# Kernel tuning notes

Hardware: AMD Instinct MI355X
Metric: run time of the kernel (lower is better)

## Reference

```python
import jax, jax.numpy as jnp
import numpy as np

H = 256      # hid_dim
HEADS = 4
DH = H // HEADS
B = 256      # batch
L = 128      # route_max_len (all routes full length)
T = 256      # max_trg_len
ID = 50000   # id_size
IN_DIM = H + 1  # emb + rate


def setup_inputs() -> dict:
    key = jax.random.key(0)
    ks = jax.random.split(key, 20)
    # bidirectional chain edges per sample, with node offsets pre-applied
    j = np.arange(L - 1)
    s = np.concatenate([j, j + 1]); d = np.concatenate([j + 1, j])
    off = (np.arange(B) * L)[:, None]
    edge_index = jnp.asarray(np.stack([(s[None] + off).reshape(-1),
                                       (d[None] + off).reshape(-1)]), dtype=jnp.int64)
    sc = 0.05
    inp = dict(
        route_emb=jax.random.normal(ks[0], (B, L, H), jnp.float32),
        edge_index=edge_index,
        trg_id=jax.random.randint(ks[1], (T, B), 0, ID),
        trg_rate=jax.random.uniform(ks[2], (T, B, 1), jnp.float32),
        routes=jax.random.randint(ks[3], (L, B), 0, ID),
        route_attn_mask=jnp.ones((B, L), jnp.int32),
        # parameters
        emb_id=jax.random.normal(ks[4], (ID, H), jnp.float32) * sc,
        gat_w=jax.random.normal(ks[5], (H, H), jnp.float32) * sc,
        gat_a_src=jax.random.normal(ks[6], (HEADS, DH), jnp.float32) * sc,
        gat_a_dst=jax.random.normal(ks[7], (HEADS, DH), jnp.float32) * sc,
        gat_bias=jnp.zeros((H,), jnp.float32),
        ln_gamma=jnp.ones((H,), jnp.float32),
        ln_beta=jnp.zeros((H,), jnp.float32),
        gru_w_ih=jax.random.normal(ks[8], (3 * H, IN_DIM), jnp.float32) * sc,
        gru_w_hh=jax.random.normal(ks[9], (3 * H, H), jnp.float32) * sc,
        gru_b_ih=jnp.zeros((3 * H,), jnp.float32),
        gru_b_hh=jnp.zeros((3 * H,), jnp.float32),
        fc1_w=jax.random.normal(ks[10], (2 * H, 2 * H), jnp.float32) * sc,
        fc1_b=jnp.zeros((2 * H,), jnp.float32),
        fc2_w=jax.random.normal(ks[11], (1, 2 * H), jnp.float32) * sc,
        fc2_b=jnp.zeros((1,), jnp.float32),
    )
    return inp


def _layernorm(x, g, b, eps=1e-5):
    m = jnp.mean(x, -1, keepdims=True)
    v = jnp.var(x, -1, keepdims=True)
    return (x - m) * jax.lax.rsqrt(v + eps) * g + b


def _gat(x, edge_index, W, a_src, a_dst, bias):
    # PyG GATConv, concat=True, add_self_loops=False, eval mode (no dropout)
    N = x.shape[0]
    xw = (x @ W).reshape(N, HEADS, DH)                   # [N,heads,dh]
    src, dst = edge_index[0], edge_index[1]
    a_s = jnp.sum(xw * a_src, -1)                        # [N,heads]
    a_d = jnp.sum(xw * a_dst, -1)
    e = a_s[src] + a_d[dst]                              # [E,heads]
    e = jnp.where(e > 0, e, 0.2 * e)                     # LeakyReLU(0.2)
    e_max = jax.ops.segment_max(e, dst, num_segments=N)
    ex = jnp.exp(e - e_max[dst])
    denom = jax.ops.segment_sum(ex, dst, num_segments=N)
    alpha = ex / (denom[dst] + 1e-16)                    # softmax per dst node
    out = jax.ops.segment_sum(xw[src] * alpha[:, :, None], dst, num_segments=N)
    return out.reshape(N, H) + bias


def _forward(route_emb, trg_rate, emb_id, gat_w, gat_a_src, gat_a_dst, gat_bias,
             ln_gamma, ln_beta, gru_w_ih, gru_w_hh, gru_b_ih, gru_b_hh,
             fc1_w, fc1_b, fc2_w, fc2_b,
             edge_index, trg_id, routes, route_attn_mask):
    # ---- RouteGraphEncoder (all routes have valid_len == L) ----
    nodes = route_emb.reshape(B * L, H)
    h_new = _gat(nodes, edge_index, gat_w, gat_a_src, gat_a_dst, gat_bias)
    h = _layernorm(nodes + h_new, ln_gamma, ln_beta)
    route_outputs = h.reshape(B, L, H)                    # [B,L,H]
    # initial decoder hidden: masked mean over route positions
    hidden0 = jnp.mean(route_outputs, axis=1)             # [B,H]

    mask = route_attn_mask                                # [B,L] int
    inv_sqrt = 1.0 / jnp.sqrt(jnp.float32(H))

    def gru_cell(x, hprev):
        gi = x @ gru_w_ih.T + gru_b_ih                    # [B,3H]
        gh = hprev @ gru_w_hh.T + gru_b_hh
        ir, iz, inn = jnp.split(gi, 3, -1)
        hr, hz, hn = jnp.split(gh, 3, -1)
        r = jax.nn.sigmoid(ir + hr)
        z = jax.nn.sigmoid(iz + hz)
        n = jnp.tanh(inn + r * hn)
        return (1.0 - z) * n + z * hprev

    def step(hprev, xs):
        tid, trate = xs                                   # [B], [B,1]
        x = jnp.concatenate([emb_id[tid], trate], -1)     # [B,H+1]
        hnew = gru_cell(x, hprev)
        scores = jnp.einsum('bh,blh->bl', hnew, route_outputs) * inv_sqrt
        scores = jnp.where(mask == 0, -1e9, scores)
        attn = jax.nn.softmax(scores, -1)                 # [B,L]
        weighted = jnp.einsum('bl,blh->bh', attn, route_outputs)
        pred_id = jnp.where(mask == 0, 0.0, attn)         # masked_fill(mask==0,0)
        rate_in = jnp.concatenate([hnew, weighted], -1)   # [B,2H]
        pred_rate = jax.nn.sigmoid(
            jax.nn.relu(rate_in @ fc1_w.T + fc1_b) @ fc2_w.T + fc2_b)  # [B,1]
        return hnew, (pred_id, pred_rate)

    # teacher forcing ratio = 1.0: input at step t is trg_id[t-1]
    xs = (trg_id[:-1], trg_rate[:-1])
    _, (ids, rates) = jax.lax.scan(step, hidden0, xs)     # [T-1,B,L],[T-1,B,1]
    outputs_id = jnp.concatenate([jnp.zeros((1, B, L), ids.dtype), ids], 0)
    outputs_rate = jnp.concatenate([jnp.zeros((1, B, 1), rates.dtype), rates], 0)
    # trg_len == T for all samples -> mask_trg is all ones (no-op)
    return outputs_id, outputs_rate


def reference(route_emb, edge_index, trg_id, trg_rate, routes, route_attn_mask,
              emb_id, gat_w, gat_a_src, gat_a_dst, gat_bias, ln_gamma, ln_beta,
              gru_w_ih, gru_w_hh, gru_b_ih, gru_b_hh, fc1_w, fc1_b, fc2_w, fc2_b):
    return _forward(route_emb, trg_rate, emb_id, gat_w, gat_a_src, gat_a_dst,
                    gat_bias, ln_gamma, ln_beta, gru_w_ih, gru_w_hh, gru_b_ih,
                    gru_b_hh, fc1_w, fc1_b, fc2_w, fc2_b,
                    edge_index, trg_id, routes, route_attn_mask)
```

## Files before the change

### kernel.cpp

```cpp
#include <hip/hip_runtime.h>
#include <math.h>

#define RATE_OFF 8388608

#define O_XW    0
#define O_SC    0
#define O_AS    8388608
#define O_AD    8519680
#define O_RO    8650752
#define O_HSEQ  17039360
#define O_H16   33882112
#define O_GI16  42303488
#define O_WE16  45449216
#define O_RACC  53805056
#define O_WIH16 53870336
#define O_FC116 53968640

typedef _Float16 half_t;
typedef __attribute__((ext_vector_type(2))) _Float16 half2_t;
typedef __attribute__((ext_vector_type(4))) _Float16 half4_t;
typedef __attribute__((ext_vector_type(8))) _Float16 half8_t;
typedef __attribute__((ext_vector_type(4))) float f32x4;

__global__ void k_misc_zero(float* __restrict__ out, float* __restrict__ racc) {
  int i = blockIdx.x * 256 + threadIdx.x;
  if (i < 32768) out[i] = 0.f;
  else if (i < 33024) out[RATE_OFF + (i - 32768)] = 0.f;
  else racc[i - 33024] = 0.f;
}

__global__ void k_cvt_w(const float* __restrict__ wih, const float* __restrict__ fc1,
                        half_t* __restrict__ wih16, half_t* __restrict__ fc116) {
  int i = blockIdx.x * 256 + threadIdx.x;
  if (i < 196608) {
    int n = i >> 8, k = i & 255;
    wih16[i] = (half_t)wih[n * 257 + k];
  } else {
    int j = i - 196608;
    fc116[j] = (half_t)fc1[j];
  }
}

__global__ __launch_bounds__(256) void k_gemm_xw(const float* __restrict__ A,
    const float* __restrict__ B, float* __restrict__ C) {
  __shared__ float As[16 * 68], Bs[16 * 68];
  const int tid = threadIdx.x;
  const int m0 = blockIdx.y * 64, n0 = blockIdx.x * 64;
  const int ty = tid >> 4, tx = tid & 15;
  const int am = tid >> 2, ak = (tid & 3) * 4;
  const int bk = tid >> 4, bn = (tid & 15) * 4;
  float c[4][4] = {};
  for (int k0 = 0; k0 < 256; k0 += 16) {
    float4 av = *(const float4*)&A[(size_t)(m0 + am) * 256 + k0 + ak];
    As[(ak + 0) * 68 + am] = av.x;
    As[(ak + 1) * 68 + am] = av.y;
    As[(ak + 2) * 68 + am] = av.z;
    As[(ak + 3) * 68 + am] = av.w;
    *(float4*)&Bs[bk * 68 + bn] = *(const float4*)&B[(size_t)(k0 + bk) * 256 + n0 + bn];
    __syncthreads();
#pragma unroll
    for (int kk = 0; kk < 16; ++kk) {
      float4 a = *(const float4*)&As[kk * 68 + ty * 4];
      float4 b = *(const float4*)&Bs[kk * 68 + tx * 4];
      float aa[4] = {a.x, a.y, a.z, a.w};
      float bb[4] = {b.x, b.y, b.z, b.w};
#pragma unroll
      for (int i = 0; i < 4; ++i)
#pragma unroll
        for (int j = 0; j < 4; ++j) c[i][j] += aa[i] * bb[j];
    }
    __syncthreads();
  }
  for (int i = 0; i < 4; ++i) {
    float4 v = make_float4(c[i][0], c[i][1], c[i][2], c[i][3]);
    *(float4*)&C[(size_t)(m0 + ty * 4 + i) * 256 + n0 + tx * 4] = v;
  }
}

__global__ void k_asd(const float* __restrict__ xw, const float* __restrict__ asrc,
                      const float* __restrict__ adst, float* __restrict__ a_s,
                      float* __restrict__ a_d) {
  int g = blockIdx.x * 256 + threadIdx.x;
  int n = g >> 2, h = g & 3;
  const float* row = &xw[(size_t)n * 256 + h * 64];
  float s1 = 0.f, s2 = 0.f;
  for (int d = 0; d < 64; ++d) {
    float v = row[d];
    s1 += v * asrc[h * 64 + d];
    s2 += v * adst[h * 64 + d];
  }
  a_s[g] = s1;
  a_d[g] = s2;
}

__global__ __launch_bounds__(256) void k_gat_ln(const float* __restrict__ xw,
    const float* __restrict__ a_s, const float* __restrict__ a_d,
    const float* __restrict__ bias, const float* __restrict__ nodes,
    const float* __restrict__ gamma, const float* __restrict__ beta,
    float* __restrict__ ro) {
  __shared__ float rs[4], rq[4];
  const int n = blockIdx.x, c = threadIdx.x, h = c >> 6;
  const int p = n & 127;
  const bool h1 = (p > 0), h2 = (p < 127);
  const float ad = a_d[n * 4 + h];
  float e1 = -1e30f, e2 = -1e30f;
  if (h1) { float e = a_s[(n - 1) * 4 + h] + ad; e1 = (e > 0.f) ? e : 0.2f * e; }
  if (h2) { float e = a_s[(n + 1) * 4 + h] + ad; e2 = (e > 0.f) ? e : 0.2f * e; }
  const float mx = fmaxf(e1, e2);
  const float x1 = h1 ? expf(e1 - mx) : 0.f;
  const float x2 = h2 ? expf(e2 - mx) : 0.f;
  const float inv = 1.f / (x1 + x2 + 1e-16f);
  float o = 0.f;
  if (h1) o += x1 * inv * xw[(size_t)(n - 1) * 256 + c];
  if (h2) o += x2 * inv * xw[(size_t)(n + 1) * 256 + c];
  o += bias[c];
  const float t = nodes[(size_t)n * 256 + c] + o;
  float sv = t, qv = t * t;
  for (int off = 32; off; off >>= 1) { sv += __shfl_down(sv, off); qv += __shfl_down(qv, off); }
  if ((c & 63) == 0) { rs[c >> 6] = sv; rq[c >> 6] = qv; }
  __syncthreads();
  const float S = rs[0] + rs[1] + rs[2] + rs[3];
  const float Q = rq[0] + rq[1] + rq[2] + rq[3];
  const float mean = S * (1.f / 256.f);
  const float var = Q * (1.f / 256.f) - mean * mean;
  ro[(size_t)n * 256 + c] = (t - mean) * rsqrtf(var + 1e-5f) * gamma[c] + beta[c];
}

__global__ void k_hidden0(const float* __restrict__ ro, float* __restrict__ hseq) {
  int b = blockIdx.x, c = threadIdx.x;
  float s = 0.f;
  for (int l = 0; l < 128; ++l) s += ro[(size_t)(b * 128 + l) * 256 + c];
  hseq[(size_t)b * 256 + c] = s * (1.f / 128.f);
}

__global__ __launch_bounds__(256) void k_gi_mfma(const float* __restrict__ emb,
    const int* __restrict__ tgid, const float* __restrict__ trate,
    const half_t* __restrict__ wih16, const float* __restrict__ wih,
    const float* __restrict__ bih, half_t* __restrict__ gi16, int s0) {
  const int tid = threadIdx.x;
  const int wave = tid >> 6, lane = tid & 63;
  const int q = lane >> 4, ln = lane & 15;
  const int m0 = blockIdx.y * 64;
  const int nw = blockIdx.x * 256 + wave * 64;
  const float* aptr[4];
#pragma unroll
  for (int mt = 0; mt < 4; ++mt) {
    const int mr = m0 + mt * 16 + ln;
    const int sl = mr >> 8, b = mr & 255;
    const int id = tgid[(s0 + sl) * 256 + b];
    aptr[mt] = emb + (size_t)id * 256;
  }
  f32x4 acc[4][4] = {};
  for (int kc = 0; kc < 8; ++kc) {
    const int k0 = kc * 32;
    const int kq = k0 + q * 8;
    half8_t a[4], bfr[4];
#pragma unroll
    for (int mt = 0; mt < 4; ++mt) {
      float4 f0 = *(const float4*)(aptr[mt] + kq);
      float4 f1 = *(const float4*)(aptr[mt] + kq + 4);
      half8_t v;
      v[0] = (half_t)f0.x; v[1] = (half_t)f0.y; v[2] = (half_t)f0.z; v[3] = (half_t)f0.w;
      v[4] = (half_t)f1.x; v[5] = (half_t)f1.y; v[6] = (half_t)f1.z; v[7] = (half_t)f1.w;
      a[mt] = v;
    }
#pragma unroll
    for (int nt = 0; nt < 4; ++nt) {
      const int n = nw + nt * 16 + ln;
      bfr[nt] = *(const half8_t*)(wih16 + (size_t)n * 256 + kq);
    }
#pragma unroll
    for (int mt = 0; mt < 4; ++mt)
#pragma unroll
      for (int nt = 0; nt < 4; ++nt)
        acc[mt][nt] = __builtin_amdgcn_mfma_f32_16x16x32_f16(a[mt], bfr[nt], acc[mt][nt], 0, 0, 0);
  }
  float wr[4], bb[4];
#pragma unroll
  for (int nt = 0; nt < 4; ++nt) {
    const int n = nw + nt * 16 + ln;
    wr[nt] = wih[(size_t)n * 257 + 256];
    bb[nt] = bih[n];
  }
#pragma unroll
  for (int mt = 0; mt < 4; ++mt) {
#pragma unroll
    for (int i = 0; i < 4; ++i) {
      const int mr2 = m0 + mt * 16 + q * 4 + i;
      const int sl = mr2 >> 8, b = mr2 & 255;
      const float tr = trate[(s0 + sl) * 256 + b];
#pragma unroll
      for (int nt = 0; nt < 4; ++nt) {
        const int n = nw + nt * 16 + ln;
        gi16[(size_t)mr2 * 768 + n] = (half_t)(acc[mt][nt][i] + tr * wr[nt] + bb[nt]);
      }
    }
  }
}

__global__ __launch_bounds__(768, 3) void k_scan(const float* __restrict__ whh,
    const half_t* __restrict__ gi16, const float* __restrict__ bhh,
    float* __restrict__ hseq, half_t* __restrict__ h16, int s0, int ns) {
  __shared__ half2_t h2[128];
  __shared__ float hf[256];
  __shared__ float gsum[768];
  const int tid = threadIdx.x;
  const int b = blockIdx.x;
  half2_t w[128];
  const float* wrow = &whh[(size_t)tid * 256];
#pragma unroll
  for (int i = 0; i < 64; ++i) {
    float4 v = *(const float4*)&wrow[i * 4];
    half2_t p0, p1;
    p0.x = (half_t)v.x; p0.y = (half_t)v.y;
    p1.x = (half_t)v.z; p1.y = (half_t)v.w;
    w[2 * i] = p0;
    w[2 * i + 1] = p1;
  }
  const float bh = bhh[tid];
  if (tid < 256) {
    float hv = hseq[(size_t)s0 * 65536 + (size_t)b * 256 + tid];
    hf[tid] = hv;
    ((half_t*)h2)[tid] = (half_t)hv;
  }
  __syncthreads();
  for (int sl = 0; sl < ns; ++sl) {
    float gr = 0.f, gz = 0.f, gn = 0.f;
    if (tid < 256) {
      const half_t* gis = &gi16[((size_t)sl * 256 + b) * 768];
      gr = (float)gis[tid]; gz = (float)gis[256 + tid]; gn = (float)gis[512 + tid];
    }
    float acc = bh;
#pragma unroll
    for (int i = 0; i < 128; ++i) {
#if __has_builtin(__builtin_amdgcn_fdot2)
      acc = __builtin_amdgcn_fdot2(h2[i], w[i], acc, false);
#else
      half2_t hv = h2[i], wv = w[i];
      acc += (float)hv.x * (float)wv.x + (float)hv.y * (float)wv.y;
#endif
    }
    gsum[tid] = acc;
    __syncthreads();
    if (tid < 256) {
      const float r = 1.f / (1.f + expf(-(gr + gsum[tid])));
      const float z = 1.f / (1.f + expf(-(gz + gsum[256 + tid])));
      const float nn = tanhf(gn + r * gsum[512 + tid]);
      const float hn = (1.f - z) * nn + z * hf[tid];
      hf[tid] = hn;
      ((half_t*)h2)[tid] = (half_t)hn;
      hseq[(size_t)(s0 + sl + 1) * 65536 + (size_t)b * 256 + tid] = hn;
      h16[(size_t)(s0 + sl + 1) * 65536 + (size_t)b * 256 + tid] = (half_t)hn;
    }
    __syncthreads();
  }
}

__global__ __launch_bounds__(256) void k_scores(const float* __restrict__ hseq,
    const float* __restrict__ ro, float* __restrict__ sc) {
  __shared__ float As[16 * 68], Bs[16 * 68];
  const int tid = threadIdx.x;
  const int l0 = blockIdx.x * 64, s0 = blockIdx.y * 64, b = blockIdx.z;
  const int ty = tid >> 4, tx = tid & 15;
  const int am = tid >> 2, ak = (tid & 3) * 4;
  const float* hrow = &hseq[(size_t)(s0 + am + 1) * 65536 + (size_t)b * 256];
  const float* brow = &ro[(size_t)b * 32768 + (size_t)(l0 + am) * 256];
  float c[4][4] = {};
  for (int k0 = 0; k0 < 256; k0 += 16) {
    float4 av = *(const float4*)&hrow[k0 + ak];
    As[(ak + 0) * 68 + am] = av.x;
    As[(ak + 1) * 68 + am] = av.y;
    As[(ak + 2) * 68 + am] = av.z;
    As[(ak + 3) * 68 + am] = av.w;
    float4 bv = *(const float4*)&brow[k0 + ak];
    Bs[(ak + 0) * 68 + am] = bv.x;
    Bs[(ak + 1) * 68 + am] = bv.y;
    Bs[(ak + 2) * 68 + am] = bv.z;
    Bs[(ak + 3) * 68 + am] = bv.w;
    __syncthreads();
#pragma unroll
    for (int kk = 0; kk < 16; ++kk) {
      float4 a = *(const float4*)&As[kk * 68 + ty * 4];
      float4 b2 = *(const float4*)&Bs[kk * 68 + tx * 4];
      float aa[4] = {a.x, a.y, a.z, a.w};
      float bb[4] = {b2.x, b2.y, b2.z, b2.w};
#pragma unroll
      for (int i = 0; i < 4; ++i)
#pragma unroll
        for (int j = 0; j < 4; ++j) c[i][j] += aa[i] * bb[j];
    }
    __syncthreads();
  }
  for (int i = 0; i < 4; ++i) {
    const int s = s0 + ty * 4 + i;
    if (s < 255) {
      float4 v = make_float4(c[i][0], c[i][1], c[i][2], c[i][3]);
      *(float4*)&sc[(size_t)b * 32640 + (size_t)s * 128 + l0 + tx * 4] = v;
    }
  }
}

__global__ void k_softmax(const int* __restrict__ mask, float* __restrict__ sc,
                          float* __restrict__ out_ids) {
  const int b = blockIdx.x, s = blockIdx.y, tid = threadIdx.x;
  float* row = &sc[(size_t)b * 32640 + (size_t)s * 128];
  float2 v = *(const float2*)&row[tid * 2];
  const int m0 = mask[b * 128 + tid * 2], m1 = mask[b * 128 + tid * 2 + 1];
  float a = (m0 == 0) ? -1e9f : v.x * 0.0625f;
  float c = (m1 == 0) ? -1e9f : v.y * 0.0625f;
  float mx = fmaxf(a, c);
  for (int off = 32; off; off >>= 1) mx = fmaxf(mx, __shfl_xor(mx, off));
  const float e0 = expf(a - mx), e1 = expf(c - mx);
  float den = e0 + e1;
  for (int off = 32; off; off >>= 1) den += __shfl_xor(den, off);
  const float dinv = 1.f / den;
  float a0 = e0 * dinv, a1 = e1 * dinv;
  if (m0 == 0) a0 = 0.f;
  if (m1 == 0) a1 = 0.f;
  *(float2*)&row[tid * 2] = make_float2(a0, a1);
  *(float2*)&out_ids[(size_t)(s + 1) * 32768 + b * 128 + tid * 2] = make_float2(a0, a1);
}

__global__ __launch_bounds__(256) void k_weighted(const float* __restrict__ sc,
    const float* __restrict__ ro, half_t* __restrict__ we16) {
  __shared__ float As[16 * 68], Bs[16 * 68];
  const int tid = threadIdx.x;
  const int n0 = blockIdx.x * 64, s0 = blockIdx.y * 64, b = blockIdx.z;
  const int ty = tid >> 4, tx = tid & 15;
  const int am = tid >> 2, ak = (tid & 3) * 4;
  const int bk = tid >> 4, bn = (tid & 15) * 4;
  const float* arow = &sc[(size_t)b * 32640 + (size_t)(s0 + am) * 128];
  float c[4][4] = {};
  for (int k0 = 0; k0 < 128; k0 += 16) {
    float4 av = *(const float4*)&arow[k0 + ak];
    As[(ak + 0) * 68 + am] = av.x;
    As[(ak + 1) * 68 + am] = av.y;
    As[(ak + 2) * 68 + am] = av.z;
    As[(ak + 3) * 68 + am] = av.w;
    *(float4*)&Bs[bk * 68 + bn] =
        *(const float4*)&ro[(size_t)b * 32768 + (size_t)(k0 + bk) * 256 + n0 + bn];
    __syncthreads();
#pragma unroll
    for (int kk = 0; kk < 16; ++kk) {
      float4 a = *(const float4*)&As[kk * 68 + ty * 4];
      float4 b2 = *(const float4*)&Bs[kk * 68 + tx * 4];
      float aa[4] = {a.x, a.y, a.z, a.w};
      float bb[4] = {b2.x, b2.y, b2.z, b2.w};
#pragma unroll
      for (int i = 0; i < 4; ++i)
#pragma unroll
        for (int j = 0; j < 4; ++j) c[i][j] += aa[i] * bb[j];
    }
    __syncthreads();
  }
  for (int i = 0; i < 4; ++i) {
    const int s = s0 + ty * 4 + i;
    if (s < 255) {
      half4_t hv;
      hv[0] = (half_t)c[i][0]; hv[1] = (half_t)c[i][1];
      hv[2] = (half_t)c[i][2]; hv[3] = (half_t)c[i][3];
      *(half4_t*)&we16[((size_t)s * 256 + b) * 256 + n0 + tx * 4] = hv;
    }
  }
}

__global__ __launch_bounds__(256) void k_fc_mfma(const half_t* __restrict__ h16,
    const half_t* __restrict__ we16, const half_t* __restrict__ fc116,
    const float* __restrict__ fc1b, const float* __restrict__ fc2w,
    float* __restrict__ racc) {
  const int tid = threadIdx.x;
  const int wave = tid >> 6, lane = tid & 63;
  const int q = lane >> 4, ln = lane & 15;
  const int m0 = blockIdx.y * 64;
  const int nw = blockIdx.x * 256 + wave * 64;
  const int s = m0 >> 8;
  const half_t* arowA[4];
  const half_t* arowB[4];
#pragma unroll
  for (int mt = 0; mt < 4; ++mt) {
    const int m = m0 + mt * 16 + ln;
    const int br = m & 255;
    arowA[mt] = h16 + (size_t)(s + 1) * 65536 + (size_t)br * 256;
    arowB[mt] = we16 + (size_t)m * 256;
  }
  f32x4 acc[4][4] = {};
  for (int kc = 0; kc < 16; ++kc) {
    const int k0 = kc * 32;
    const int kq = (k0 & 255) + q * 8;
    const bool first = k0 < 256;
    half8_t a[4], bfr[4];
#pragma unroll
    for (int mt = 0; mt < 4; ++mt)
      a[mt] = *(const half8_t*)((first ? arowA[mt] : arowB[mt]) + kq);
#pragma unroll
    for (int nt = 0; nt < 4; ++nt) {
      const int n = nw + nt * 16 + ln;
      bfr[nt] = *(const half8_t*)(fc116 + (size_t)n * 512 + k0 + q * 8);
    }
#pragma unroll
    for (int mt = 0; mt < 4; ++mt)
#pragma unroll
      for (int nt = 0; nt < 4; ++nt)
        acc[mt][nt] = __builtin_amdgcn_mfma_f32_16x16x32_f16(a[mt], bfr[nt], acc[mt][nt], 0, 0, 0);
  }
  float fb[4], f2[4];
#pragma unroll
  for (int nt = 0; nt < 4; ++nt) {
    const int n = nw + nt * 16 + ln;
    fb[nt] = fc1b[n];
    f2[nt] = fc2w[n];
  }
#pragma unroll
  for (int mt = 0; mt < 4; ++mt) {
#pragma unroll
    for (int i = 0; i < 4; ++i) {
      float v = 0.f;
#pragma unroll
      for (int nt = 0; nt < 4; ++nt) {
        float x = acc[mt][nt][i] + fb[nt];
        v += fmaxf(x, 0.f) * f2[nt];
      }
      v += __shfl_xor(v, 1);
      v += __shfl_xor(v, 2);
      v += __shfl_xor(v, 4);
      v += __shfl_xor(v, 8);
      if (ln == 0) atomicAdd(&racc[m0 + mt * 16 + q * 4 + i], v);
    }
  }
}

__global__ void k_rate_out(const float* __restrict__ racc, const float* __restrict__ fc2b,
                           float* __restrict__ out) {
  int m = blockIdx.x * 256 + threadIdx.x;
  int s = m >> 8, b = m & 255;
  float v = racc[m] + fc2b[0];
  out[RATE_OFF + (s + 1) * 256 + b] = 1.f / (1.f + expf(-v));
}

extern "C" void kernel_launch(void* const* d_in, const int* in_sizes, int n_in,
                              void* d_out, int out_size, void* d_ws, size_t ws_size,
                              hipStream_t stream) {
  (void)in_sizes; (void)n_in; (void)out_size; (void)ws_size;
  const float* route_emb = (const float*)d_in[0];
  const int*   trg_id    = (const int*)d_in[2];
  const float* trg_rate  = (const float*)d_in[3];
  const int*   mask      = (const int*)d_in[5];
  const float* emb_id    = (const float*)d_in[6];
  const float* gat_w     = (const float*)d_in[7];
  const float* a_src     = (const float*)d_in[8];
  const float* a_dst     = (const float*)d_in[9];
  const float* gat_b     = (const float*)d_in[10];
  const float* ln_g      = (const float*)d_in[11];
  const float* ln_b      = (const float*)d_in[12];
  const float* w_ih      = (const float*)d_in[13];
  const float* w_hh      = (const float*)d_in[14];
  const float* b_ih      = (const float*)d_in[15];
  const float* b_hh      = (const float*)d_in[16];
  const float* fc1_w     = (const float*)d_in[17];
  const float* fc1_b     = (const float*)d_in[18];
  const float* fc2_w     = (const float*)d_in[19];
  const float* fc2_b     = (const float*)d_in[20];
  float* out = (float*)d_out;
  float* ws  = (float*)d_ws;
  half_t* h16   = (half_t*)(ws + O_H16);
  half_t* gi16  = (half_t*)(ws + O_GI16);
  half_t* we16  = (half_t*)(ws + O_WE16);
  half_t* wih16 = (half_t*)(ws + O_WIH16);
  half_t* fc116 = (half_t*)(ws + O_FC116);

  k_misc_zero<<<384, 256, 0, stream>>>(out, ws + O_RACC);
  k_cvt_w<<<1792, 256, 0, stream>>>(w_ih, fc1_w, wih16, fc116);
  k_gemm_xw<<<dim3(4, 512), 256, 0, stream>>>(route_emb, gat_w, ws + O_XW);
  k_asd<<<512, 256, 0, stream>>>(ws + O_XW, a_src, a_dst, ws + O_AS, ws + O_AD);
  k_gat_ln<<<32768, 256, 0, stream>>>(ws + O_XW, ws + O_AS, ws + O_AD, gat_b,
                                      route_emb, ln_g, ln_b, ws + O_RO);
  k_hidden0<<<256, 256, 0, stream>>>(ws + O_RO, ws + O_HSEQ);
  for (int cc = 0; cc < 8; ++cc) {
    int s0 = cc * 32;
    int ns = (255 - s0 < 32) ? (255 - s0) : 32;
    k_gi_mfma<<<dim3(3, ns * 4), 256, 0, stream>>>(emb_id, trg_id, trg_rate,
                                                   wih16, w_ih, b_ih, gi16, s0);
    k_scan<<<256, 768, 0, stream>>>(w_hh, gi16, b_hh, ws + O_HSEQ, h16, s0, ns);
  }
  k_scores<<<dim3(2, 4, 256), 256, 0, stream>>>(ws + O_HSEQ, ws + O_RO, ws + O_SC);
  k_softmax<<<dim3(256, 255), 64, 0, stream>>>(mask, ws + O_SC, out);
  k_weighted<<<dim3(4, 4, 256), 256, 0, stream>>>(ws + O_SC, ws + O_RO, we16);
  k_fc_mfma<<<dim3(2, 1020), 256, 0, stream>>>(h16, we16, fc116, fc1_b,
                                               fc2_w, ws + O_RACC);
  k_rate_out<<<255, 256, 0, stream>>>(ws + O_RACC, fc2_b, out);
}
```

Measured before the change: 1.581 ms.

## Run GRU scan as one kernel with three gate rows per thread

Computes all input-gate projections in one GEMM launch over the full sequence instead of eight chunks, and replaces the chunked 768-thread scan with a single 256-thread-per-batch scan. In the new scan each thread holds three W_hh rows in registers and computes its own r/z/n gates, which removes the shared-memory gate exchange and one barrier exchange per step. The fp32 hidden sequence is dropped in favour of fp16 h everywhere, and the scores kernel now reads that fp16 copy. The fc GEMM also stages its A rows in LDS. The cost is heavy register pressure (384 half2 weights per thread), lower occupancy, and less precise hidden states feeding the scores.

```diff
diff --git a/kernel.cpp b/kernel.cpp
--- a/kernel.cpp
+++ b/kernel.cpp
@@ -3,18 +3,17 @@
 
 #define RATE_OFF 8388608
 
-#define O_XW    0
-#define O_SC    0
-#define O_AS    8388608
-#define O_AD    8519680
-#define O_RO    8650752
-#define O_HSEQ  17039360
-#define O_H16   33882112
-#define O_GI16  42303488
-#define O_WE16  45449216
-#define O_RACC  53805056
-#define O_WIH16 53870336
-#define O_FC116 53968640
+#define O_A     0
+#define O_XW    O_A
+#define O_SC    O_A
+#define O_AS    25067520
+#define O_AD    25198592
+#define O_RO    25329664
+#define O_H16   33718272
+#define O_WE16  42139648
+#define O_RACC  50495488
+#define O_WIH16 50560768
+#define O_FC116 50659072
 
 typedef _Float16 half_t;
 typedef __attribute__((ext_vector_type(2))) _Float16 half2_t;
@@ -126,17 +125,17 @@
   ro[(size_t)n * 256 + c] = (t - mean) * rsqrtf(var + 1e-5f) * gamma[c] + beta[c];
 }
 
-__global__ void k_hidden0(const float* __restrict__ ro, float* __restrict__ hseq) {
+__global__ void k_hidden0(const float* __restrict__ ro, half_t* __restrict__ h16) {
   int b = blockIdx.x, c = threadIdx.x;
   float s = 0.f;
   for (int l = 0; l < 128; ++l) s += ro[(size_t)(b * 128 + l) * 256 + c];
-  hseq[(size_t)b * 256 + c] = s * (1.f / 128.f);
+  h16[(size_t)b * 256 + c] = (half_t)(s * (1.f / 128.f));
 }
 
 __global__ __launch_bounds__(256) void k_gi_mfma(const float* __restrict__ emb,
     const int* __restrict__ tgid, const float* __restrict__ trate,
     const half_t* __restrict__ wih16, const float* __restrict__ wih,
-    const float* __restrict__ bih, half_t* __restrict__ gi16, int s0) {
+    const float* __restrict__ bih, half_t* __restrict__ gi16) {
   const int tid = threadIdx.x;
   const int wave = tid >> 6, lane = tid & 63;
   const int q = lane >> 4, ln = lane & 15;
@@ -147,13 +146,12 @@
   for (int mt = 0; mt < 4; ++mt) {
     const int mr = m0 + mt * 16 + ln;
     const int sl = mr >> 8, b = mr & 255;
-    const int id = tgid[(s0 + sl) * 256 + b];
+    const int id = tgid[sl * 256 + b];
     aptr[mt] = emb + (size_t)id * 256;
   }
   f32x4 acc[4][4] = {};
   for (int kc = 0; kc < 8; ++kc) {
-    const int k0 = kc * 32;
-    const int kq = k0 + q * 8;
+    const int kq = kc * 32 + q * 8;
     half8_t a[4], bfr[4];
 #pragma unroll
     for (int mt = 0; mt < 4; ++mt) {
@@ -188,7 +186,7 @@
     for (int i = 0; i < 4; ++i) {
       const int mr2 = m0 + mt * 16 + q * 4 + i;
       const int sl = mr2 >> 8, b = mr2 & 255;
-      const float tr = trate[(s0 + sl) * 256 + b];
+      const float tr = trate[sl * 256 + b];
 #pragma unroll
       for (int nt = 0; nt < 4; ++nt) {
         const int n = nw + nt * 16 + ln;
@@ -198,80 +196,83 @@
   }
 }
 
-__global__ __launch_bounds__(768, 3) void k_scan(const float* __restrict__ whh,
+__global__ __launch_bounds__(256, 1) void k_scan2(const float* __restrict__ whh,
     const half_t* __restrict__ gi16, const float* __restrict__ bhh,
-    float* __restrict__ hseq, half_t* __restrict__ h16, int s0, int ns) {
+    half_t* __restrict__ h16) {
   __shared__ half2_t h2[128];
-  __shared__ float hf[256];
-  __shared__ float gsum[768];
   const int tid = threadIdx.x;
   const int b = blockIdx.x;
-  half2_t w[128];
-  const float* wrow = &whh[(size_t)tid * 256];
+  half2_t w0[128], w1[128], w2[128];
+  const float* r0 = whh + (size_t)tid * 256;
+  const float* r1 = whh + (size_t)(256 + tid) * 256;
+  const float* r2 = whh + (size_t)(512 + tid) * 256;
 #pragma unroll
   for (int i = 0; i < 64; ++i) {
-    float4 v = *(const float4*)&wrow[i * 4];
-    half2_t p0, p1;
-    p0.x = (half_t)v.x; p0.y = (half_t)v.y;
-    p1.x = (half_t)v.z; p1.y = (half_t)v.w;
-    w[2 * i] = p0;
-    w[2 * i + 1] = p1;
-  }
-  const float bh = bhh[tid];
-  if (tid < 256) {
-    float hv = hseq[(size_t)s0 * 65536 + (size_t)b * 256 + tid];
-    hf[tid] = hv;
-    ((half_t*)h2)[tid] = (half_t)hv;
-  }
+    float4 v0 = *(const float4*)&r0[i * 4];
+    float4 v1 = *(const float4*)&r1[i * 4];
+    float4 v2 = *(const float4*)&r2[i * 4];
+    half2_t p;
+    p.x = (half_t)v0.x; p.y = (half_t)v0.y; w0[2 * i] = p;
+    p.x = (half_t)v0.z; p.y = (half_t)v0.w; w0[2 * i + 1] = p;
+    p.x = (half_t)v1.x; p.y = (half_t)v1.y; w1[2 * i] = p;
+    p.x = (half_t)v1.z; p.y = (half_t)v1.w; w1[2 * i + 1] = p;
+    p.x = (half_t)v2.x; p.y = (half_t)v2.y; w2[2 * i] = p;
+    p.x = (half_t)v2.z; p.y = (half_t)v2.w; w2[2 * i + 1] = p;
+  }
+  const float bh0 = bhh[tid], bh1 = bhh[256 + tid], bh2 = bhh[512 + tid];
+  float hprev = (float)h16[(size_t)b * 256 + tid];
+  ((half_t*)h2)[tid] = (half_t)hprev;
   __syncthreads();
-  for (int sl = 0; sl < ns; ++sl) {
-    float gr = 0.f, gz = 0.f, gn = 0.f;
-    if (tid < 256) {
-      const half_t* gis = &gi16[((size_t)sl * 256 + b) * 768];
-      gr = (float)gis[tid]; gz = (float)gis[256 + tid]; gn = (float)gis[512 + tid];
-    }
-    float acc = bh;
-#pragma unroll
-    for (int i = 0; i < 128; ++i) {
+  for (int sl = 0; sl < 255; ++sl) {
+    const half_t* gis = &gi16[((size_t)sl * 256 + b) * 768];
+    const float gr = (float)gis[tid];
+    const float gz = (float)gis[256 + tid];
+    const float gn = (float)gis[512 + tid];
+    float a0 = bh0, a1 = bh1, a2 = bh2;
+#pragma unroll
+    for (int c = 0; c < 16; ++c) {
+#pragma unroll
+      for (int j = 0; j < 8; ++j) {
+        const half2_t hv = h2[c * 8 + j];
 #if __has_builtin(__builtin_amdgcn_fdot2)
-      acc = __builtin_amdgcn_fdot2(h2[i], w[i], acc, false);
+        a0 = __builtin_amdgcn_fdot2(hv, w0[c * 8 + j], a0, false);
+        a1 = __builtin_amdgcn_fdot2(hv, w1[c * 8 + j], a1, false);
+        a2 = __builtin_amdgcn_fdot2(hv, w2[c * 8 + j], a2, false);
 #else
-      half2_t hv = h2[i], wv = w[i];
-      acc += (float)hv.x * (float)wv.x + (float)hv.y * (float)wv.y;
+        a0 += (float)hv.x * (float)w0[c * 8 + j].x + (float)hv.y * (float)w0[c * 8 + j].y;
+        a1 += (float)hv.x * (float)w1[c * 8 + j].x + (float)hv.y * (float)w1[c * 8 + j].y;
+        a2 += (float)hv.x * (float)w2[c * 8 + j].x + (float)hv.y * (float)w2[c * 8 + j].y;
 #endif
-    }
-    gsum[tid] = acc;
-    __syncthreads();
-    if (tid < 256) {
-      const float r = 1.f / (1.f + expf(-(gr + gsum[tid])));
-      const float z = 1.f / (1.f + expf(-(gz + gsum[256 + tid])));
-      const float nn = tanhf(gn + r * gsum[512 + tid]);
-      const float hn = (1.f - z) * nn + z * hf[tid];
-      hf[tid] = hn;
-      ((half_t*)h2)[tid] = (half_t)hn;
-      hseq[(size_t)(s0 + sl + 1) * 65536 + (size_t)b * 256 + tid] = hn;
-      h16[(size_t)(s0 + sl + 1) * 65536 + (size_t)b * 256 + tid] = (half_t)hn;
-    }
-    __syncthreads();
-  }
-}
-
-__global__ __launch_bounds__(256) void k_scores(const float* __restrict__ hseq,
+      }
+    }
+    const float r = 1.f / (1.f + expf(-(gr + a0)));
+    const float z = 1.f / (1.f + expf(-(gz + a1)));
+    const float nn = tanhf(gn + r * a2);
+    const float hn = (1.f - z) * nn + z * hprev;
+    hprev = hn;
+    __syncthreads();
+    ((half_t*)h2)[tid] = (half_t)hn;
+    h16[(size_t)(sl + 1) * 65536 + (size_t)b * 256 + tid] = (half_t)hn;
+    __syncthreads();
+  }
+}
+
+__global__ __launch_bounds__(256) void k_scores(const half_t* __restrict__ h16,
     const float* __restrict__ ro, float* __restrict__ sc) {
   __shared__ float As[16 * 68], Bs[16 * 68];
   const int tid = threadIdx.x;
   const int l0 = blockIdx.x * 64, s0 = blockIdx.y * 64, b = blockIdx.z;
   const int ty = tid >> 4, tx = tid & 15;
   const int am = tid >> 2, ak = (tid & 3) * 4;
-  const float* hrow = &hseq[(size_t)(s0 + am + 1) * 65536 + (size_t)b * 256];
+  const half_t* hrow = &h16[(size_t)(s0 + am + 1) * 65536 + (size_t)b * 256];
   const float* brow = &ro[(size_t)b * 32768 + (size_t)(l0 + am) * 256];
   float c[4][4] = {};
   for (int k0 = 0; k0 < 256; k0 += 16) {
-    float4 av = *(const float4*)&hrow[k0 + ak];
-    As[(ak + 0) * 68 + am] = av.x;
-    As[(ak + 1) * 68 + am] = av.y;
-    As[(ak + 2) * 68 + am] = av.z;
-    As[(ak + 3) * 68 + am] = av.w;
+    half4_t hv4 = *(const half4_t*)&hrow[k0 + ak];
+    As[(ak + 0) * 68 + am] = (float)hv4[0];
+    As[(ak + 1) * 68 + am] = (float)hv4[1];
+    As[(ak + 2) * 68 + am] = (float)hv4[2];
+    As[(ak + 3) * 68 + am] = (float)hv4[3];
     float4 bv = *(const float4*)&brow[k0 + ak];
     Bs[(ak + 0) * 68 + am] = bv.x;
     Bs[(ak + 1) * 68 + am] = bv.y;
@@ -368,34 +369,35 @@
     const half_t* __restrict__ we16, const half_t* __restrict__ fc116,
     const float* __restrict__ fc1b, const float* __restrict__ fc2w,
     float* __restrict__ racc) {
-  const int tid = threadIdx.x;
+  __shared__ half_t Als[64 * 520];
+  const int tid = threadIdx.x;
+  const int m0 = blockIdx.y * 64;
+  const int s = m0 >> 8;
+#pragma unroll
+  for (int it = 0; it < 16; ++it) {
+    const int u = it * 256 + tid;
+    const int row = u >> 6, ch = u & 63;
+    const int m = m0 + row, br = m & 255;
+    const half_t* src = (ch < 32)
+        ? h16 + (size_t)(s + 1) * 65536 + (size_t)br * 256 + ch * 8
+        : we16 + (size_t)m * 256 + (size_t)(ch - 32) * 8;
+    *(half8_t*)&Als[row * 520 + ch * 8] = *(const half8_t*)src;
+  }
+  __syncthreads();
   const int wave = tid >> 6, lane = tid & 63;
   const int q = lane >> 4, ln = lane & 15;
-  const int m0 = blockIdx.y * 64;
   const int nw = blockIdx.x * 256 + wave * 64;
-  const int s = m0 >> 8;
-  const half_t* arowA[4];
-  const half_t* arowB[4];
-#pragma unroll
-  for (int mt = 0; mt < 4; ++mt) {
-    const int m = m0 + mt * 16 + ln;
-    const int br = m & 255;
-    arowA[mt] = h16 + (size_t)(s + 1) * 65536 + (size_t)br * 256;
-    arowB[mt] = we16 + (size_t)m * 256;
-  }
   f32x4 acc[4][4] = {};
   for (int kc = 0; kc < 16; ++kc) {
-    const int k0 = kc * 32;
-    const int kq = (k0 & 255) + q * 8;
-    const bool first = k0 < 256;
+    const int kq = kc * 32 + q * 8;
     half8_t a[4], bfr[4];
 #pragma unroll
     for (int mt = 0; mt < 4; ++mt)
-      a[mt] = *(const half8_t*)((first ? arowA[mt] : arowB[mt]) + kq);
+      a[mt] = *(const half8_t*)&Als[(mt * 16 + ln) * 520 + kq];
 #pragma unroll
     for (int nt = 0; nt < 4; ++nt) {
       const int n = nw + nt * 16 + ln;
-      bfr[nt] = *(const half8_t*)(fc116 + (size_t)n * 512 + k0 + q * 8);
+      bfr[nt] = *(const half8_t*)(fc116 + (size_t)n * 512 + kq);
     }
 #pragma unroll
     for (int mt = 0; mt < 4; ++mt)
@@ -462,8 +464,8 @@
   const float* fc2_b     = (const float*)d_in[20];
   float* out = (float*)d_out;
   float* ws  = (float*)d_ws;
+  half_t* gi16  = (half_t*)(ws + O_A);
   half_t* h16   = (half_t*)(ws + O_H16);
-  half_t* gi16  = (half_t*)(ws + O_GI16);
   half_t* we16  = (half_t*)(ws + O_WE16);
   half_t* wih16 = (half_t*)(ws + O_WIH16);
   half_t* fc116 = (half_t*)(ws + O_FC116);
@@ -474,15 +476,11 @@
   k_asd<<<512, 256, 0, stream>>>(ws + O_XW, a_src, a_dst, ws + O_AS, ws + O_AD);
   k_gat_ln<<<32768, 256, 0, stream>>>(ws + O_XW, ws + O_AS, ws + O_AD, gat_b,
                                       route_emb, ln_g, ln_b, ws + O_RO);
-  k_hidden0<<<256, 256, 0, stream>>>(ws + O_RO, ws + O_HSEQ);
-  for (int cc = 0; cc < 8; ++cc) {
-    int s0 = cc * 32;
-    int ns = (255 - s0 < 32) ? (255 - s0) : 32;
-    k_gi_mfma<<<dim3(3, ns * 4), 256, 0, stream>>>(emb_id, trg_id, trg_rate,
-                                                   wih16, w_ih, b_ih, gi16, s0);
-    k_scan<<<256, 768, 0, stream>>>(w_hh, gi16, b_hh, ws + O_HSEQ, h16, s0, ns);
-  }
-  k_scores<<<dim3(2, 4, 256), 256, 0, stream>>>(ws + O_HSEQ, ws + O_RO, ws + O_SC);
+  k_hidden0<<<256, 256, 0, stream>>>(ws + O_RO, h16);
+  k_gi_mfma<<<dim3(3, 1020), 256, 0, stream>>>(emb_id, trg_id, trg_rate,
+                                               wih16, w_ih, b_ih, gi16);
+  k_scan2<<<256, 256, 0, stream>>>(w_hh, gi16, b_hh, h16);
+  k_scores<<<dim3(2, 4, 256), 256, 0, stream>>>(h16, ws + O_RO, ws + O_SC);
   k_softmax<<<dim3(256, 255), 64, 0, stream>>>(mask, ws + O_SC, out);
   k_weighted<<<dim3(4, 4, 256), 256, 0, stream>>>(ws + O_SC, ws + O_RO, we16);
   k_fc_mfma<<<dim3(2, 1020), 256, 0, stream>>>(h16, we16, fc116, fc1_b,
```

Result: no change. 1.608 ms (+1.7%).
